# Kernel optimization log

Hardware: AMD Instinct MI355X
Metric: run time of the kernel (lower is better)

Reference implementation:

```python
import jax, jax.numpy as jnp
import numpy as np

LOAD_BALANCE_WEIGHT = 0.05


def setup_inputs() -> dict:
    key = jax.random.key(0)
    ks = jax.random.split(key, 8)
    B, H, C, E = 8192, 4096, 1000, 4
    s_h = 1.0 / np.sqrt(H)
    return {
        "x": jax.random.normal(ks[0], (B, H), dtype=jnp.float32),
        "Wr": jax.random.normal(ks[1], (H, E), dtype=jnp.float32) * s_h,
        "br": jnp.zeros((E,), dtype=jnp.float32),
        "W1": jax.random.normal(ks[2], (E, H, H), dtype=jnp.float32) * s_h,
        "b1": jnp.zeros((E, H), dtype=jnp.float32),
        "W2": jax.random.normal(ks[3], (E, H, C), dtype=jnp.float32) * s_h,
        "b2": jnp.zeros((E, C), dtype=jnp.float32),
    }


def reference(x, Wr, br, W1, b1, W2, b2):
    # Router: linear gate -> softmax probs (eval mode: no noise)
    E = Wr.shape[1]
    router_logits = x @ Wr + br                     # [B, E]
    routing_weights = jax.nn.softmax(router_logits, axis=-1)
    # Hard top-1 dispatch
    idx = jnp.argmax(routing_weights, axis=-1)      # [B]
    onehot = jax.nn.one_hot(idx, E, dtype=x.dtype)  # [B, E]
    # Switch-style load-balance loss: E * sum(fraction_e * mean_prob_e)
    frac = onehot.mean(axis=0)                      # [E]
    mean_p = routing_weights.mean(axis=0)           # [E]
    load_balance_loss = LOAD_BALANCE_WEIGHT * E * jnp.sum(frac * mean_p)
    # Dense all-expert compute, then hard-select per token (same math as
    # gather/scatter dispatch in the torch loop, fully vectorized)
    h = jax.nn.gelu(jnp.einsum('bh,ehk->ebk', x, W1) + b1[:, None, :])  # [E,B,H]
    expert_out = jnp.einsum('ebk,ekc->ebc', h, W2) + b2[:, None, :]     # [E,B,C]
    logits = jnp.einsum('be,ebc->bc', onehot, expert_out)               # [B,C]
    return logits, load_balance_loss, routing_weights
```

## Files before the change

### kernel.cpp

```cpp
#include <hip/hip_runtime.h>
#include <hip/hip_bf16.h>

#define NB 8192
#define NH 4096
#define NC 1000
#define NE 4
#define NCP 1024

typedef __attribute__((ext_vector_type(4))) float f32x4;
typedef __attribute__((ext_vector_type(8))) short s16x8;
typedef __attribute__((ext_vector_type(4))) unsigned int u32x4;

__device__ __forceinline__ unsigned cvtpk(float a, float b){
  unsigned r; asm("v_cvt_pk_bf16_f32 %0, %1, %2" : "=v"(r) : "v"(a), "v"(b)); return r;
}
__device__ __forceinline__ int swz_off(int r, int s){
  return (r << 6) + (((s ^ (r ^ (r >> 2))) & 3) << 4);
}

__device__ __forceinline__ void gload16(const void* g, void* l) {
  __builtin_amdgcn_global_load_lds(
      (const __attribute__((address_space(1))) unsigned int*)g,
      (__attribute__((address_space(3))) unsigned int*)l, 16, 0, 0);
}

__global__ __launch_bounds__(256) void router2_k(
    const float* __restrict__ x, const float* __restrict__ Wr,
    const float* __restrict__ br, float* __restrict__ out,
    int* __restrict__ idx, int* __restrict__ cnt_part, float* __restrict__ sum_part,
    __hip_bfloat16* __restrict__ xb)
{
  int b = blockIdx.x, t = threadIdx.x;
  const float* xr = x + (size_t)b * NH;
  int h0 = t << 4;
  f32x4 v[4];
  #pragma unroll
  for (int j = 0; j < 4; j++) v[j] = *(const f32x4*)(xr + h0 + (j << 2));
  u32x4 ob0 = { cvtpk(v[0][0],v[0][1]), cvtpk(v[0][2],v[0][3]),
                cvtpk(v[1][0],v[1][1]), cvtpk(v[1][2],v[1][3]) };
  u32x4 ob1 = { cvtpk(v[2][0],v[2][1]), cvtpk(v[2][2],v[2][3]),
                cvtpk(v[3][0],v[3][1]), cvtpk(v[3][2],v[3][3]) };
  *(u32x4*)(xb + (size_t)b * NH + h0) = ob0;
  *(u32x4*)(xb + (size_t)b * NH + h0 + 8) = ob1;

  double a0=0, a1=0, a2=0, a3=0;
  #pragma unroll
  for (int i = 0; i < 16; i++) {
    float xv = v[i >> 2][i & 3];
    f32x4 w = *(const f32x4*)(Wr + (size_t)(h0 + i) * 4);
    double xd = (double)xv;
    a0 += xd * (double)w[0]; a1 += xd * (double)w[1];
    a2 += xd * (double)w[2]; a3 += xd * (double)w[3];
  }
  for (int off = 32; off; off >>= 1) {
    a0 += __shfl_down(a0, off); a1 += __shfl_down(a1, off);
    a2 += __shfl_down(a2, off); a3 += __shfl_down(a3, off);
  }
  __shared__ double red[4][4];
  int wid = t >> 6;
  if ((t & 63) == 0) { red[wid][0]=a0; red[wid][1]=a1; red[wid][2]=a2; red[wid][3]=a3; }
  __syncthreads();
  if (t == 0) {
    double l[4];
    for (int e = 0; e < 4; e++)
      l[e] = red[0][e] + red[1][e] + red[2][e] + red[3][e] + (double)br[e];
    int am = 0; double mx = l[0];
    for (int e = 1; e < 4; e++) if (l[e] > mx) { mx = l[e]; am = e; }
    double p[4], s = 0;
    for (int e = 0; e < 4; e++) { p[e] = exp(l[e] - mx); s += p[e]; }
    float* rw = out + (size_t)NB * NC + 1 + (size_t)b * 4;
    int bin = (b & 63) * 4;
    for (int e = 0; e < 4; e++) {
      float pe = (float)(p[e] / s);
      rw[e] = pe;
      atomicAdd(&sum_part[bin + e], pe);
    }
    idx[b] = am;
    atomicAdd(&cnt_part[bin + am], 1);
  }
}

__global__ __launch_bounds__(256) void router_k(
    const float* __restrict__ x, const float* __restrict__ Wr,
    const float* __restrict__ br, float* __restrict__ out,
    int* __restrict__ idx, int* __restrict__ cnt_part, float* __restrict__ sum_part)
{
  int b = blockIdx.x, t = threadIdx.x;
  const float* xr = x + (size_t)b * NH;
  double a0=0, a1=0, a2=0, a3=0;
  for (int i = 0; i < 16; i++) {
    int h = t + (i << 8);
    float xv = xr[h];
    f32x4 w = *(const f32x4*)(Wr + (size_t)h * 4);
    double xd = (double)xv;
    a0 += xd * (double)w[0]; a1 += xd * (double)w[1];
    a2 += xd * (double)w[2]; a3 += xd * (double)w[3];
  }
  for (int off = 32; off; off >>= 1) {
    a0 += __shfl_down(a0, off); a1 += __shfl_down(a1, off);
    a2 += __shfl_down(a2, off); a3 += __shfl_down(a3, off);
  }
  __shared__ double red[4][4];
  int wid = t >> 6;
  if ((t & 63) == 0) { red[wid][0]=a0; red[wid][1]=a1; red[wid][2]=a2; red[wid][3]=a3; }
  __syncthreads();
  if (t == 0) {
    double l[4];
    for (int e = 0; e < 4; e++)
      l[e] = red[0][e] + red[1][e] + red[2][e] + red[3][e] + (double)br[e];
    int am = 0; double mx = l[0];
    for (int e = 1; e < 4; e++) if (l[e] > mx) { mx = l[e]; am = e; }
    double p[4], s = 0;
    for (int e = 0; e < 4; e++) { p[e] = exp(l[e] - mx); s += p[e]; }
    float* rw = out + (size_t)NB * NC + 1 + (size_t)b * 4;
    int bin = (b & 63) * 4;
    for (int e = 0; e < 4; e++) {
      float pe = (float)(p[e] / s);
      rw[e] = pe;
      atomicAdd(&sum_part[bin + e], pe);
    }
    idx[b] = am;
    atomicAdd(&cnt_part[bin + am], 1);
  }
}

__global__ void finalize_k(const int* __restrict__ cnt_part, const float* __restrict__ sum_part,
                           int* __restrict__ counts, int* __restrict__ offs, float* __restrict__ out)
{
  int t = threadIdx.x;
  __shared__ int cc[4]; __shared__ float ss[4];
  if (t < 4) {
    int c = 0; float s = 0;
    for (int i = 0; i < 64; i++) { c += cnt_part[i*4 + t]; s += sum_part[i*4 + t]; }
    cc[t] = c; ss[t] = s; counts[t] = c;
  }
  __syncthreads();
  if (t == 0) {
    int o = 0; float loss = 0.f;
    for (int e = 0; e < 4; e++) {
      offs[e] = o; o += cc[e];
      loss += ((float)cc[e] / (float)NB) * (ss[e] / (float)NB);
    }
    out[(size_t)NB * NC] = 0.05f * (float)NE * loss;
  }
}

__global__ __launch_bounds__(256) void scatter_k(
    const int* __restrict__ idx, const int* __restrict__ offs,
    int* __restrict__ cursors, int* __restrict__ perm)
{
  int b = blockIdx.x * 256 + threadIdx.x;
  int e = idx[b];
  int lane = threadIdx.x & 63;
  for (int e2 = 0; e2 < 4; e2++) {
    unsigned long long m = __ballot(e == e2);
    if (e == e2) {
      int nbelow = __popcll(m & ((1ULL << lane) - 1ULL));
      int base = 0;
      if (nbelow == 0) base = atomicAdd(&cursors[e2], (int)__popcll(m));
      int src = __ffsll((long long)m) - 1;
      base = __shfl(base, src);
      perm[offs[e2] + base + nbelow] = b;
    }
  }
}

__global__ __launch_bounds__(256) void transpose_k(
    const float* __restrict__ in, __hip_bfloat16* __restrict__ outp,
    int R, int C, int Cout)
{
  int e = blockIdx.z;
  int r0 = blockIdx.y << 5;
  int c0 = blockIdx.x << 10;
  const float* ine = in + (size_t)e * R * C;
  __hip_bfloat16* oute = outp + (size_t)e * Cout * R;
  int t = threadIdx.x;
  int c = c0 + (t << 2);
  unsigned o[4][16];
  if (c < C) {
    #pragma unroll
    for (int rp = 0; rp < 16; rp++) {
      f32x4 v0 = *(const f32x4*)(ine + (size_t)(r0 + 2*rp)     * C + c);
      f32x4 v1 = *(const f32x4*)(ine + (size_t)(r0 + 2*rp + 1) * C + c);
      #pragma unroll
      for (int j = 0; j < 4; j++) o[j][rp] = cvtpk(v0[j], v1[j]);
    }
  } else {
    #pragma unroll
    for (int j = 0; j < 4; j++)
      #pragma unroll
      for (int rp = 0; rp < 16; rp++) o[j][rp] = 0;
  }
  #pragma unroll
  for (int j = 0; j < 4; j++) {
    u32x4* dst = (u32x4*)(oute + (size_t)(c + j) * R + r0);
    dst[0] = (u32x4){ o[j][0],  o[j][1],  o[j][2],  o[j][3]  };
    dst[1] = (u32x4){ o[j][4],  o[j][5],  o[j][6],  o[j][7]  };
    dst[2] = (u32x4){ o[j][8],  o[j][9],  o[j][10], o[j][11] };
    dst[3] = (u32x4){ o[j][12], o[j][13], o[j][14], o[j][15] };
  }
}


#define DSR(off) (*(const s16x8*)(lds + (off)))

template<int MODE>
__global__ __launch_bounds__(256, 3) void gemmsb_k(
    const __hip_bfloat16* __restrict__ Ax, const __hip_bfloat16* __restrict__ Bw,
    const float* __restrict__ bias, const int* __restrict__ perm,
    const int* __restrict__ counts, const int* __restrict__ offs,
    __hip_bfloat16* __restrict__ H1out, float* __restrict__ out)
{
  int e = blockIdx.z;
  int cnt = counts[e];
  if (cnt == 0) return;
  int m0 = blockIdx.y << 7;
  if (m0 >= cnt) return;
  int seg = offs[e];
  int n0 = blockIdx.x << 7;
  const __hip_bfloat16* Be = Bw + (size_t)e * (size_t)(MODE == 0 ? NH : NCP) * NH;

  __shared__ __align__(16) char lds[32768];
  __shared__ int rowtok[128];

  int tid = threadIdx.x;
  if (tid < 128) {
    int rr = m0 + tid; if (rr >= cnt) rr = cnt - 1;
    rowtok[tid] = perm[seg + rr];
  }
  __syncthreads();

  int lane = tid & 63, w = tid >> 6;
  int wr = w >> 1, wc = w & 1;
  int cx = lane & 15, g = lane >> 4;
  int l8 = lane >> 3, l7 = lane & 7;

  int srcoff = (l7 ^ l8) << 3;
  const __hip_bfloat16* pA[4];
  const __hip_bfloat16* pB[4];
  #pragma unroll
  for (int i = 0; i < 4; i++) {
    int r = w * 32 + i * 8 + l8;
    if constexpr (MODE == 0) {
      pA[i] = Ax + (size_t)rowtok[r] * NH + srcoff;
    } else {
      int rr = m0 + r; if (rr >= cnt) rr = cnt - 1;
      pA[i] = Ax + (size_t)(seg + rr) * NH + srcoff;
    }
    pB[i] = Be + (size_t)(n0 + r) * NH + srcoff;
  }
  int wst = w * 4096;

  int swz0 = ((0 * 4 + g) ^ (cx & 7)) << 4;
  int swz1 = ((1 * 4 + g) ^ (cx & 7)) << 4;
  int arow = (wr * 64 + cx) * 128;
  int brow = (wc * 64 + cx) * 128;

  f32x4 acc[4][4] = {};

  const int NT = NH / 64;

  for (int t = 0; t < NT; t++) {
    gload16(pA[0] + (size_t)t*64, lds + wst);
    gload16(pA[1] + (size_t)t*64, lds + wst + 1024);
    gload16(pA[2] + (size_t)t*64, lds + wst + 2048);
    gload16(pA[3] + (size_t)t*64, lds + wst + 3072);
    gload16(pB[0] + (size_t)t*64, lds + 16384 + wst);
    gload16(pB[1] + (size_t)t*64, lds + 16384 + wst + 1024);
    gload16(pB[2] + (size_t)t*64, lds + 16384 + wst + 2048);
    gload16(pB[3] + (size_t)t*64, lds + 16384 + wst + 3072);
    __syncthreads();

    s16x8 a0_[4], b0_[4], a1_[4], b1_[4];
    #pragma unroll
    for (int mf = 0; mf < 4; mf++) a0_[mf] = DSR(arow + mf*2048 + swz0);
    #pragma unroll
    for (int nf = 0; nf < 4; nf++) b0_[nf] = DSR(16384 + brow + nf*2048 + swz0);
    #pragma unroll
    for (int mf = 0; mf < 4; mf++)
      #pragma unroll
      for (int nf = 0; nf < 4; nf++)
        acc[mf][nf] = __builtin_amdgcn_mfma_f32_16x16x32_bf16(a0_[mf], b0_[nf], acc[mf][nf], 0, 0, 0);
    #pragma unroll
    for (int mf = 0; mf < 4; mf++) a1_[mf] = DSR(arow + mf*2048 + swz1);
    #pragma unroll
    for (int nf = 0; nf < 4; nf++) b1_[nf] = DSR(16384 + brow + nf*2048 + swz1);
    #pragma unroll
    for (int mf = 0; mf < 4; mf++)
      #pragma unroll
      for (int nf = 0; nf < 4; nf++)
        acc[mf][nf] = __builtin_amdgcn_mfma_f32_16x16x32_bf16(a1_[mf], b1_[nf], acc[mf][nf], 0, 0, 0);
    __syncthreads();
  }

  #pragma unroll
  for (int nf = 0; nf < 4; nf++) {
    int n = n0 + wc * 64 + nf * 16 + cx;
    if (MODE == 0 || n < NC) {
      float bv = bias[(size_t)e * (MODE == 0 ? NH : NC) + n];
      #pragma unroll
      for (int mf = 0; mf < 4; mf++) {
        f32x4 vacc = acc[mf][nf];
        #pragma unroll
        for (int i = 0; i < 4; i++) {
          int mrow = wr * 64 + mf * 16 + g * 4 + i;
          int mseg = m0 + mrow;
          if (mseg < cnt) {
            float u = vacc[i] + bv;
            if constexpr (MODE == 0) {
              float th = tanhf(0.79788456080286535588f * (u + 0.044715f * u * u * u));
              float hv = 0.5f * u * (1.0f + th);
              H1out[(size_t)(seg + mseg) * NH + n] = __float2bfloat16(hv);
            } else {
              int tok = rowtok[mrow];
              out[(size_t)tok * NC + n] = u;
            }
          }
        }
      }
    }
  }
}

__global__ __launch_bounds__(256) void gemm1_k(
    const float* __restrict__ x, const float* __restrict__ W1,
    const float* __restrict__ b1, const int* __restrict__ perm,
    const int* __restrict__ counts, const int* __restrict__ offs,
    __hip_bfloat16* __restrict__ H1)
{
  int e = blockIdx.z;
  int cnt = counts[e];
  int m0 = blockIdx.y << 7;
  if (m0 >= cnt) return;
  int seg = offs[e];
  int n0 = blockIdx.x << 7;
  const float* W1e = W1 + (size_t)e * NH * NH;

  __shared__ __align__(16) char As[128*32*2];
  __shared__ __align__(16) char Bs[128*32*2];
  __shared__ int rowtok[128];

  int t = threadIdx.x;
  if (t < 128) {
    int rr = m0 + t; if (rr >= cnt) rr = cnt - 1;
    rowtok[t] = perm[seg + rr];
  }
  __syncthreads();

  int ar0 = t >> 2, as_ = t & 3;
  int ar1 = ar0 + 64;
  const float* asrc0 = x + (size_t)rowtok[ar0] * NH + (as_ << 3);
  const float* asrc1 = x + (size_t)rowtok[ar1] * NH + (as_ << 3);
  int aw0 = swz_off(ar0, as_), aw1 = swz_off(ar1, as_);
  int bnc = t & 31, bkp = t >> 5;
  const float* bsrc0 = W1e + (size_t)(bkp << 1) * NH + n0 + (bnc << 2);
  const float* bsrc1 = bsrc0 + (size_t)16 * NH;

  f32x4 acc[4][4] = {};

  int lane = t & 63, wid = t >> 6;
  int wm = (wid >> 1) << 6, wn = (wid & 1) << 6;
  int g = lane >> 4, cx = lane & 15;
  int aoff[4], boff[4];
  #pragma unroll
  for (int f = 0; f < 4; f++) {
    aoff[f] = swz_off(wm + (f << 4) + cx, g);
    boff[f] = swz_off(wn + (f << 4) + cx, g);
  }

  for (int kt = 0; kt < NH; kt += 32) {
    {
      f32x4 v0 = *(const f32x4*)(asrc0 + kt);
      f32x4 v1 = *(const f32x4*)(asrc0 + kt + 4);
      u32x4 wv = { cvtpk(v0[0],v0[1]), cvtpk(v0[2],v0[3]), cvtpk(v1[0],v1[1]), cvtpk(v1[2],v1[3]) };
      *(u32x4*)(As + aw0) = wv;
      f32x4 u0 = *(const f32x4*)(asrc1 + kt);
      f32x4 u1 = *(const f32x4*)(asrc1 + kt + 4);
      u32x4 w2 = { cvtpk(u0[0],u0[1]), cvtpk(u0[2],u0[3]), cvtpk(u1[0],u1[1]), cvtpk(u1[2],u1[3]) };
      *(u32x4*)(As + aw1) = w2;
    }
    {
      const float* p0 = bsrc0 + (size_t)kt * NH;
      f32x4 rr0 = *(const f32x4*)p0;
      f32x4 rr1 = *(const f32x4*)(p0 + NH);
      int kp = bkp, sl = kp >> 2, sub = (kp & 3) << 2;
      #pragma unroll
      for (int j = 0; j < 4; j++) {
        int n = (bnc << 2) + j;
        *(unsigned*)(Bs + (n << 6) + (((sl ^ (n ^ (n >> 2))) & 3) << 4) + sub) = cvtpk(rr0[j], rr1[j]);
      }
      const float* p1 = bsrc1 + (size_t)kt * NH;
      f32x4 q0 = *(const f32x4*)p1;
      f32x4 q1 = *(const f32x4*)(p1 + NH);
      kp = bkp + 8; sl = kp >> 2; sub = (kp & 3) << 2;
      #pragma unroll
      for (int j = 0; j < 4; j++) {
        int n = (bnc << 2) + j;
        *(unsigned*)(Bs + (n << 6) + (((sl ^ (n ^ (n >> 2))) & 3) << 4) + sub) = cvtpk(q0[j], q1[j]);
      }
    }
    __syncthreads();
    s16x8 af[4], bfr[4];
    #pragma unroll
    for (int f = 0; f < 4; f++) {
      af[f]  = *(const s16x8*)(As + aoff[f]);
      bfr[f] = *(const s16x8*)(Bs + boff[f]);
    }
    #pragma unroll
    for (int mf = 0; mf < 4; mf++)
      #pragma unroll
      for (int nf = 0; nf < 4; nf++)
        acc[mf][nf] = __builtin_amdgcn_mfma_f32_16x16x32_bf16(af[mf], bfr[nf], acc[mf][nf], 0, 0, 0);
    __syncthreads();
  }

  const float* b1e = b1 + (size_t)e * NH;
  #pragma unroll
  for (int nf = 0; nf < 4; nf++) {
    int n = n0 + wn + (nf << 4) + cx;
    float bv = b1e[n];
    #pragma unroll
    for (int mf = 0; mf < 4; mf++) {
      #pragma unroll
      for (int i = 0; i < 4; i++) {
        int mseg = m0 + wm + (mf << 4) + (g << 2) + i;
        if (mseg < cnt) {
          float u = acc[mf][nf][i] + bv;
          float th = tanhf(0.79788456080286535588f * (u + 0.044715f * u * u * u));
          float hv = 0.5f * u * (1.0f + th);
          H1[(size_t)(seg + mseg) * NH + n] = __float2bfloat16(hv);
        }
      }
    }
  }
}

__global__ __launch_bounds__(256) void gemm2_k(
    const __hip_bfloat16* __restrict__ H1, const float* __restrict__ W2,
    const float* __restrict__ b2, const int* __restrict__ perm,
    const int* __restrict__ counts, const int* __restrict__ offs,
    float* __restrict__ out)
{
  int e = blockIdx.z;
  int cnt = counts[e];
  int m0 = blockIdx.y << 7;
  if (m0 >= cnt) return;
  int seg = offs[e];
  int n0 = blockIdx.x << 7;
  const float* W2e = W2 + (size_t)e * NH * NC;

  __shared__ __align__(16) char As[128*32*2];
  __shared__ __align__(16) char Bs[128*32*2];
  __shared__ int rowtok[128];

  int t = threadIdx.x;
  if (t < 128) {
    int rr = m0 + t; if (rr >= cnt) rr = cnt - 1;
    rowtok[t] = perm[seg + rr];
  }
  __syncthreads();

  int ar0 = t >> 2, as_ = t & 3;
  int ar1 = ar0 + 64;
  int rA0 = m0 + ar0; if (rA0 >= cnt) rA0 = cnt - 1;
  int rA1 = m0 + ar1; if (rA1 >= cnt) rA1 = cnt - 1;
  const __hip_bfloat16* asrc0 = H1 + (size_t)(seg + rA0) * NH + (as_ << 3);
  const __hip_bfloat16* asrc1 = H1 + (size_t)(seg + rA1) * NH + (as_ << 3);
  int aw0 = swz_off(ar0, as_), aw1 = swz_off(ar1, as_);

  int bnc = t & 31, bkp = t >> 5;
  int col = n0 + (bnc << 2);
  bool bvalid = col < NC;
  const float* bsrc0 = W2e + (size_t)(bkp << 1) * NC + col;
  const float* bsrc1 = bsrc0 + (size_t)16 * NC;

  f32x4 acc[4][4] = {};

  int lane = t & 63, wid = t >> 6;
  int wm = (wid >> 1) << 6, wn = (wid & 1) << 6;
  int g = lane >> 4, cx = lane & 15;
  int aoff[4], boff[4];
  #pragma unroll
  for (int f = 0; f < 4; f++) {
    aoff[f] = swz_off(wm + (f << 4) + cx, g);
    boff[f] = swz_off(wn + (f << 4) + cx, g);
  }

  for (int kt = 0; kt < NH; kt += 32) {
    {
      *(u32x4*)(As + aw0) = *(const u32x4*)(asrc0 + kt);
      *(u32x4*)(As + aw1) = *(const u32x4*)(asrc1 + kt);
    }
    {
      f32x4 rr0 = {}, rr1 = {}, q0 = {}, q1 = {};
      if (bvalid) {
        const float* p0 = bsrc0 + (size_t)kt * NC;
        rr0 = *(const f32x4*)p0; rr1 = *(const f32x4*)(p0 + NC);
        const float* p1 = bsrc1 + (size_t)kt * NC;
        q0 = *(const f32x4*)p1; q1 = *(const f32x4*)(p1 + NC);
      }
      int kp = bkp, sl = kp >> 2, sub = (kp & 3) << 2;
      #pragma unroll
      for (int j = 0; j < 4; j++) {
        int n = (bnc << 2) + j;
        *(unsigned*)(Bs + (n << 6) + (((sl ^ (n ^ (n >> 2))) & 3) << 4) + sub) = cvtpk(rr0[j], rr1[j]);
      }
      kp = bkp + 8; sl = kp >> 2; sub = (kp & 3) << 2;
      #pragma unroll
      for (int j = 0; j < 4; j++) {
        int n = (bnc << 2) + j;
        *(unsigned*)(Bs + (n << 6) + (((sl ^ (n ^ (n >> 2))) & 3) << 4) + sub) = cvtpk(q0[j], q1[j]);
      }
    }
    __syncthreads();
    s16x8 af[4], bfr[4];
    #pragma unroll
    for (int f = 0; f < 4; f++) {
      af[f]  = *(const s16x8*)(As + aoff[f]);
      bfr[f] = *(const s16x8*)(Bs + boff[f]);
    }
    #pragma unroll
    for (int mf = 0; mf < 4; mf++)
      #pragma unroll
      for (int nf = 0; nf < 4; nf++)
        acc[mf][nf] = __builtin_amdgcn_mfma_f32_16x16x32_bf16(af[mf], bfr[nf], acc[mf][nf], 0, 0, 0);
    __syncthreads();
  }

  const float* b2e = b2 + (size_t)e * NC;
  #pragma unroll
  for (int nf = 0; nf < 4; nf++) {
    int n = n0 + wn + (nf << 4) + cx;
    if (n < NC) {
      float bv = b2e[n];
      #pragma unroll
      for (int mf = 0; mf < 4; mf++) {
        #pragma unroll
        for (int i = 0; i < 4; i++) {
          int mseg = m0 + wm + (mf << 4) + (g << 2) + i;
          if (mseg < cnt) {
            int tok = rowtok[wm + (mf << 4) + (g << 2) + i];
            out[(size_t)tok * NC + n] = acc[mf][nf][i] + bv;
          }
        }
      }
    }
  }
}

extern "C" void kernel_launch(void* const* d_in, const int* in_sizes, int n_in,
                              void* d_out, int out_size, void* d_ws, size_t ws_size,
                              hipStream_t stream) {
  const float* x  = (const float*)d_in[0];
  const float* Wr = (const float*)d_in[1];
  const float* br = (const float*)d_in[2];
  const float* W1 = (const float*)d_in[3];
  const float* b1 = (const float*)d_in[4];
  const float* W2 = (const float*)d_in[5];
  const float* b2 = (const float*)d_in[6];
  float* out = (float*)d_out;

  char* ws = (char*)d_ws;
  const size_t SZ_XB  = (size_t)NB * NH * 2;
  const size_t SZ_H1  = (size_t)NB * NH * 2;
  const size_t SZ_W1T = (size_t)NE * NH * NH * 2;
  const size_t SZ_W2T = (size_t)NE * NCP * NH * 2;
  const size_t need = SZ_XB + SZ_H1 + SZ_W1T + SZ_W2T + (size_t)NB*4*2 + 4096;

  if (ws_size >= need) {
    size_t o = 0;
    __hip_bfloat16* xb  = (__hip_bfloat16*)(ws + o); o += SZ_XB;
    __hip_bfloat16* H1  = (__hip_bfloat16*)(ws + o); o += SZ_H1;
    __hip_bfloat16* W1t = (__hip_bfloat16*)(ws + o); o += SZ_W1T;
    __hip_bfloat16* W2t = (__hip_bfloat16*)(ws + o); o += SZ_W2T;
    int* idx  = (int*)(ws + o); o += (size_t)NB * 4;
    int* perm = (int*)(ws + o); o += (size_t)NB * 4;
    char* small = ws + o;
    int*   cursors  = (int*)(small);
    int*   counts   = (int*)(small + 16);
    int*   offs     = (int*)(small + 32);
    int*   cnt_part = (int*)(small + 64);
    float* sum_part = (float*)(small + 64 + 1024);

    hipMemsetAsync(small, 0, 64 + 2048, stream);
    transpose_k<<<dim3(4, 128, 4), 256, 0, stream>>>(W1, W1t, NH, NH, NH);
    transpose_k<<<dim3(1, 128, 4), 256, 0, stream>>>(W2, W2t, NH, NC, NCP);
    router2_k<<<NB, 256, 0, stream>>>(x, Wr, br, out, idx, cnt_part, sum_part, xb);
    finalize_k<<<1, 64, 0, stream>>>(cnt_part, sum_part, counts, offs, out);
    scatter_k<<<NB / 256, 256, 0, stream>>>(idx, offs, cursors, perm);
    gemmsb_k<0><<<dim3(32, 64, 4), 256, 0, stream>>>(xb, W1t, b1, perm, counts, offs, H1, nullptr);
    gemmsb_k<1><<<dim3(8, 64, 4), 256, 0, stream>>>(H1, W2t, b2, perm, counts, offs, nullptr, out);
  } else {
    __hip_bfloat16* H1 = (__hip_bfloat16*)ws;
    size_t o = (size_t)NB * NH * 2;
    int* idx  = (int*)(ws + o); o += (size_t)NB * 4;
    int* perm = (int*)(ws + o); o += (size_t)NB * 4;
    char* small = ws + o;
    int*   cursors  = (int*)(small);
    int*   counts   = (int*)(small + 16);
    int*   offs     = (int*)(small + 32);
    int*   cnt_part = (int*)(small + 64);
    float* sum_part = (float*)(small + 64 + 1024);

    hipMemsetAsync(small, 0, 64 + 2048, stream);
    router_k<<<NB, 256, 0, stream>>>(x, Wr, br, out, idx, cnt_part, sum_part);
    finalize_k<<<1, 64, 0, stream>>>(cnt_part, sum_part, counts, offs, out);
    scatter_k<<<NB / 256, 256, 0, stream>>>(idx, offs, cursors, perm);
    gemm1_k<<<dim3(32, 64, 4), 256, 0, stream>>>(x, W1, b1, perm, counts, offs, H1);
    gemm2_k<<<dim3(8, 64, 4), 256, 0, stream>>>(H1, W2, b2, perm, counts, offs, out);
  }
}
```

Measured before the change: 746.9 us.

## Fuse weight transposes and router into one prep kernel, remap GEMM tiles

Merges the two weight-transpose launches and the router/bf16-conversion launch into a single prep kernel whose block index selects the role, cutting launch gaps and letting the independent pieces overlap. The grouped GEMM now remaps flat workgroup IDs into a strided order so that workgroups dispatched around the same time, which are likely spread across XCDs, pick different tiles, aiming for better L2 reuse. The launch-bounds occupancy hint rises from 3 to 4 waves per SIMD, which may force register spills.

```diff
diff --git a/kernel.cpp b/kernel.cpp
--- a/kernel.cpp
+++ b/kernel.cpp
@@ -24,13 +24,59 @@
       (__attribute__((address_space(3))) unsigned int*)l, 16, 0, 0);
 }
 
-__global__ __launch_bounds__(256) void router2_k(
+__device__ __forceinline__ void transpose_body(
+    const float* __restrict__ ine, __hip_bfloat16* __restrict__ oute,
+    int R, int C, int r0, int c0, int t)
+{
+  int c = c0 + (t << 2);
+  unsigned o[4][16];
+  if (c < C) {
+    #pragma unroll
+    for (int rp = 0; rp < 16; rp++) {
+      f32x4 v0 = *(const f32x4*)(ine + (size_t)(r0 + 2*rp)     * C + c);
+      f32x4 v1 = *(const f32x4*)(ine + (size_t)(r0 + 2*rp + 1) * C + c);
+      #pragma unroll
+      for (int j = 0; j < 4; j++) o[j][rp] = cvtpk(v0[j], v1[j]);
+    }
+  } else {
+    #pragma unroll
+    for (int j = 0; j < 4; j++)
+      #pragma unroll
+      for (int rp = 0; rp < 16; rp++) o[j][rp] = 0;
+  }
+  #pragma unroll
+  for (int j = 0; j < 4; j++) {
+    u32x4* dst = (u32x4*)(oute + (size_t)(c + j) * R + r0);
+    dst[0] = (u32x4){ o[j][0],  o[j][1],  o[j][2],  o[j][3]  };
+    dst[1] = (u32x4){ o[j][4],  o[j][5],  o[j][6],  o[j][7]  };
+    dst[2] = (u32x4){ o[j][8],  o[j][9],  o[j][10], o[j][11] };
+    dst[3] = (u32x4){ o[j][12], o[j][13], o[j][14], o[j][15] };
+  }
+}
+
+__global__ __launch_bounds__(256) void prep_k(
     const float* __restrict__ x, const float* __restrict__ Wr,
     const float* __restrict__ br, float* __restrict__ out,
     int* __restrict__ idx, int* __restrict__ cnt_part, float* __restrict__ sum_part,
-    __hip_bfloat16* __restrict__ xb)
-{
-  int b = blockIdx.x, t = threadIdx.x;
+    __hip_bfloat16* __restrict__ xb,
+    const float* __restrict__ W1, __hip_bfloat16* __restrict__ W1t,
+    const float* __restrict__ W2, __hip_bfloat16* __restrict__ W2t)
+{
+  int blk = blockIdx.x, t = threadIdx.x;
+  if (blk < 2048) {
+    int e = blk >> 9, by = (blk >> 2) & 127, bx = blk & 3;
+    transpose_body(W1 + (size_t)e * NH * NH, W1t + (size_t)e * NH * NH,
+                   NH, NH, by << 5, bx << 10, t);
+    return;
+  }
+  if (blk < 2560) {
+    int bb = blk - 2048;
+    int e = bb >> 7, by = bb & 127;
+    transpose_body(W2 + (size_t)e * NH * NC, W2t + (size_t)e * NCP * NH,
+                   NH, NC, by << 5, 0, t);
+    return;
+  }
+  int b = blk - 2560;
   const float* xr = x + (size_t)b * NH;
   int h0 = t << 4;
   f32x4 v[4];
@@ -170,42 +216,15 @@
     int R, int C, int Cout)
 {
   int e = blockIdx.z;
-  int r0 = blockIdx.y << 5;
-  int c0 = blockIdx.x << 10;
-  const float* ine = in + (size_t)e * R * C;
-  __hip_bfloat16* oute = outp + (size_t)e * Cout * R;
-  int t = threadIdx.x;
-  int c = c0 + (t << 2);
-  unsigned o[4][16];
-  if (c < C) {
-    #pragma unroll
-    for (int rp = 0; rp < 16; rp++) {
-      f32x4 v0 = *(const f32x4*)(ine + (size_t)(r0 + 2*rp)     * C + c);
-      f32x4 v1 = *(const f32x4*)(ine + (size_t)(r0 + 2*rp + 1) * C + c);
-      #pragma unroll
-      for (int j = 0; j < 4; j++) o[j][rp] = cvtpk(v0[j], v1[j]);
-    }
-  } else {
-    #pragma unroll
-    for (int j = 0; j < 4; j++)
-      #pragma unroll
-      for (int rp = 0; rp < 16; rp++) o[j][rp] = 0;
-  }
-  #pragma unroll
-  for (int j = 0; j < 4; j++) {
-    u32x4* dst = (u32x4*)(oute + (size_t)(c + j) * R + r0);
-    dst[0] = (u32x4){ o[j][0],  o[j][1],  o[j][2],  o[j][3]  };
-    dst[1] = (u32x4){ o[j][4],  o[j][5],  o[j][6],  o[j][7]  };
-    dst[2] = (u32x4){ o[j][8],  o[j][9],  o[j][10], o[j][11] };
-    dst[3] = (u32x4){ o[j][12], o[j][13], o[j][14], o[j][15] };
-  }
+  transpose_body(in + (size_t)e * R * C, outp + (size_t)e * Cout * R,
+                 R, C, blockIdx.y << 5, blockIdx.x << 10, threadIdx.x);
 }
 
 
 #define DSR(off) (*(const s16x8*)(lds + (off)))
 
 template<int MODE>
-__global__ __launch_bounds__(256, 3) void gemmsb_k(
+__global__ __launch_bounds__(256, 4) void gemmsb_k(
     const __hip_bfloat16* __restrict__ Ax, const __hip_bfloat16* __restrict__ Bw,
     const float* __restrict__ bias, const int* __restrict__ perm,
     const int* __restrict__ counts, const int* __restrict__ offs,
@@ -214,10 +233,19 @@
   int e = blockIdx.z;
   int cnt = counts[e];
   if (cnt == 0) return;
-  int m0 = blockIdx.y << 7;
+
+  const int NX = (MODE == 0 ? 32 : 8);
+  const int NWG = NX * 64;
+  const int CPX = NWG / 8;
+  int flat = blockIdx.x + NX * blockIdx.y;
+  int lg = (flat & 7) * CPX + (flat >> 3);
+  int by = lg & 63;
+  int bx = lg >> 6;
+
+  int m0 = by << 7;
   if (m0 >= cnt) return;
   int seg = offs[e];
-  int n0 = blockIdx.x << 7;
+  int n0 = bx << 7;
   const __hip_bfloat16* Be = Bw + (size_t)e * (size_t)(MODE == 0 ? NH : NCP) * NH;
 
   __shared__ __align__(16) char lds[32768];
@@ -583,9 +611,8 @@
     float* sum_part = (float*)(small + 64 + 1024);
 
     hipMemsetAsync(small, 0, 64 + 2048, stream);
-    transpose_k<<<dim3(4, 128, 4), 256, 0, stream>>>(W1, W1t, NH, NH, NH);
-    transpose_k<<<dim3(1, 128, 4), 256, 0, stream>>>(W2, W2t, NH, NC, NCP);
-    router2_k<<<NB, 256, 0, stream>>>(x, Wr, br, out, idx, cnt_part, sum_part, xb);
+    prep_k<<<10752, 256, 0, stream>>>(x, Wr, br, out, idx, cnt_part, sum_part, xb,
+                                      W1, W1t, W2, W2t);
     finalize_k<<<1, 64, 0, stream>>>(cnt_part, sum_part, counts, offs, out);
     scatter_k<<<NB / 256, 256, 0, stream>>>(idx, offs, cursors, perm);
     gemmsb_k<0><<<dim3(32, 64, 4), 256, 0, stream>>>(xb, W1t, b1, perm, counts, offs, H1, nullptr);
```

Result: no change. 750.6 us (+0.5%).
